# Performance work log

Hardware: AMD Instinct MI355X
Metric: run time of the kernel (lower is better)

The kernel has to match this reference:

```python
import jax, jax.numpy as jnp
import numpy as np


def _ln(x, g, b, eps=1e-5):
    mu = x.mean(-1, keepdims=True)
    var = ((x - mu) ** 2).mean(-1, keepdims=True)
    return (x - mu) / jnp.sqrt(var + eps) * g + b


def setup_inputs() -> dict:
    key = jax.random.key(0)
    ks = jax.random.split(key, 12)
    B, H, W, nh = 32, 64, 64, 8
    L = H * W
    dim, ffn_dim, mem_dim = 512, 2048, 512
    s = 0.02
    d = {}
    d["query"] = jax.random.normal(ks[0], (B, 1, dim), jnp.float32)
    d["mem"] = jax.random.normal(ks[1], (B, L, mem_dim), jnp.float32)
    d["ior_embs"] = jax.random.uniform(ks[2], (B, nh, H, W), jnp.float32)
    # input_proj: Linear(mem_dim, dim) + ReLU + LayerNorm(dim)
    d["W_in"] = jax.random.normal(ks[3], (mem_dim, dim), jnp.float32) * s
    d["b_in"] = jnp.zeros((dim,), jnp.float32)
    d["g_in"] = jnp.ones((dim,), jnp.float32)
    d["be_in"] = jnp.zeros((dim,), jnp.float32)
    # q_w: Linear(dim, dim); kv_w: Linear(dim, 2*dim)
    d["Wq"] = jax.random.normal(ks[4], (dim, dim), jnp.float32) * s
    d["bq"] = jnp.zeros((dim,), jnp.float32)
    d["Wkv"] = jax.random.normal(ks[5], (dim, 2 * dim), jnp.float32) * s
    d["bkv"] = jnp.zeros((2 * dim,), jnp.float32)
    # ffn: Mlp(dim, ffn_dim, dim) with GELU (exact)
    d["W1"] = jax.random.normal(ks[6], (dim, ffn_dim), jnp.float32) * s
    d["b1"] = jnp.zeros((ffn_dim,), jnp.float32)
    d["W2"] = jax.random.normal(ks[7], (ffn_dim, dim), jnp.float32) * s
    d["b2"] = jnp.zeros((dim,), jnp.float32)
    # norm_q, norm_ffn LayerNorms
    d["g_q"] = jnp.ones((dim,), jnp.float32)
    d["be_q"] = jnp.zeros((dim,), jnp.float32)
    d["g_f"] = jnp.ones((dim,), jnp.float32)
    d["be_f"] = jnp.zeros((dim,), jnp.float32)
    return d


def reference(query, mem, ior_embs, W_in, b_in, g_in, be_in, Wq, bq, Wkv, bkv,
              W1, b1, W2, b2, g_q, be_q, g_f, be_f):
    # input_proj: Linear + ReLU + LayerNorm
    m = _ln(jax.nn.relu(mem @ W_in + b_in), g_in, be_in)  # [B,L,C]
    B, L, C = m.shape
    nh = ior_embs.shape[1]
    h = C // nh
    scale = h ** -0.5
    ior = ior_embs.reshape(B, nh, L)  # flatten(2)
    kv = m @ Wkv + bkv
    k, v = kv[..., :C], kv[..., C:]
    # per-head split along last dim == reshape to [.., nh, h]
    q = (_ln(query, g_q, be_q) @ Wq + bq).reshape(B, 1, nh, h)
    k = k.reshape(B, L, nh, h)
    v = v.reshape(B, L, nh, h)
    # softmax-free attention gated by ior mask: attn = (q@k^T)*scale*ior
    attn = jnp.einsum('bqhd,blhd->bhql', q, k) * scale * ior[:, :, None, :]  # [B,nh,1,L]
    x = jnp.einsum('bhql,blhd->bqhd', attn, v).reshape(B, 1, C)  # concat heads
    x = x + query  # residual (short_cut)
    # FFN with pre-norm; dropout p=0 -> identity
    hdn = jax.nn.gelu(_ln(x, g_f, be_f) @ W1 + b1, approximate=False)
    x = x + (hdn @ W2 + b2)
    return x
```

## Files before the change

kernel.cpp:

```cpp
#include <hip/hip_runtime.h>
#include <hip/hip_bf16.h>
#include <math.h>

typedef unsigned short u16;
typedef __bf16 bf16x8 __attribute__((ext_vector_type(8)));
typedef float f32x4 __attribute__((ext_vector_type(4)));

__device__ __forceinline__ float b2f(u16 u) {
  union { unsigned int i; float f; } v; v.i = ((unsigned int)u) << 16; return v.f;
}
__device__ __forceinline__ u16 f2b(float f) {
  union { float f; unsigned int i; } v; v.f = f;
  unsigned int x = v.i;
  return (u16)((x + 0x7fffu + ((x >> 16) & 1u)) >> 16);
}
__device__ __forceinline__ float ldx(const void* p, size_t i, int isf) {
  return isf ? ((const float*)p)[i] : b2f(((const u16*)p)[i]);
}

__global__ void k_detect(const void* __restrict__ query, int* __restrict__ flag) {
  int t = threadIdx.x;
  float v = ((const float*)query)[t];
  int ok = (v == v && fabsf(v) < 100.f && fabsf(v) > 1e-4f) ? 1 : 0;
  unsigned long long m = __ballot(ok);
  if (t == 0) flag[0] = (__popcll(m) >= 32) ? 1 : 0;
}

__global__ __launch_bounds__(256) void k_makeB(const void* __restrict__ Win,
                                               u16* __restrict__ WTf,
                                               const int* __restrict__ flag) {
  int isf = flag[0];
  int t = threadIdx.x;
  int bx = blockIdx.x & 7, by = blockIdx.x >> 3;
  int k0 = bx * 64, j0 = by * 64;
  __shared__ float tile[64][65];
  #pragma unroll
  for (int kx = 0; kx < 16; kx++) {
    int idx = t + 256 * kx;
    int kl = idx >> 6, jl = idx & 63;
    tile[kl][jl] = ldx(Win, (size_t)(k0 + kl) * 512 + (j0 + jl), isf);
  }
  __syncthreads();
  #pragma unroll
  for (int i = 0; i < 2; i++) {
    int chunk = i * 256 + t;
    int q  = chunk & 3;
    int l  = (chunk >> 2) & 15;
    int ksL = (chunk >> 6) & 1;
    int jbL = (chunk >> 7) & 3;
    int j_local = jbL * 16 + l;
    int k_local = ksL * 32 + q * 8;
    union { u16 h[8]; uint4 u; } pk;
    #pragma unroll
    for (int r = 0; r < 8; r++) pk.h[r] = f2b(tile[k_local + r][j_local]);
    int jb = by * 4 + jbL, ks = bx * 2 + ksL;
    *(uint4*)(WTf + ((size_t)(jb * 16 + ks) * 16 + l) * 32 + q * 8) = pk.u;
  }
}

__global__ __launch_bounds__(512) void k_prep2(const void* __restrict__ Wkv,
                                               const void* __restrict__ g_in,
                                               const void* __restrict__ be_in,
                                               float* __restrict__ P1, float* __restrict__ P2,
                                               const int* __restrict__ flag) {
  int isf = flag[0];
  int blk = blockIdx.x;
  int t = threadIdx.x;
  int jj = t & 31, cg = t >> 5;
  int j = blk * 32 + jj;
  float p1 = 0.f, p2 = 0.f;
  for (int cc = 0; cc < 32; cc++) {
    int c = cg * 32 + cc;
    float wv = ldx(Wkv, (size_t)c * 1024 + 512 + j, isf);
    p1 += ldx(g_in, c, isf) * wv;
    p2 += ldx(be_in, c, isf) * wv;
  }
  __shared__ float red[1024];
  red[t * 2] = p1; red[t * 2 + 1] = p2;
  __syncthreads();
  if (t < 32) {
    float s1 = 0.f, s2 = 0.f;
    for (int g2 = 0; g2 < 16; g2++) { s1 += red[(g2 * 32 + t) * 2]; s2 += red[(g2 * 32 + t) * 2 + 1]; }
    P1[blk * 32 + t] = s1;
    P2[blk * 32 + t] = s2;
  }
}

__global__ __launch_bounds__(256) void k_qprep_a(
    const void* __restrict__ query, const void* __restrict__ Wq, const void* __restrict__ bq,
    const void* __restrict__ g_q, const void* __restrict__ be_q,
    float* __restrict__ qr_ws, const int* __restrict__ flag) {
  int isf = flag[0];
  int b = blockIdx.x, jq = blockIdx.y, t = threadIdx.x;
  __shared__ float qf[512];
  __shared__ float red[8];
  __shared__ float stats[2];

  float s = 0.f, ss = 0.f;
  for (int k = 0; k < 2; k++) {
    int c = t + 256 * k;
    float v = ldx(query, (size_t)b * 512 + c, isf);
    qf[c] = v; s += v; ss += v * v;
  }
  for (int off = 32; off; off >>= 1) { s += __shfl_xor(s, off); ss += __shfl_xor(ss, off); }
  int wid = t >> 6, lane = t & 63;
  if (lane == 0) { red[wid * 2] = s; red[wid * 2 + 1] = ss; }
  __syncthreads();
  if (t == 0) {
    float S = 0.f, SS = 0.f;
    for (int w = 0; w < 4; w++) { S += red[w * 2]; SS += red[w * 2 + 1]; }
    float mu = S / 512.f;
    float var = SS / 512.f - mu * mu;
    stats[0] = mu; stats[1] = rsqrtf(var + 1e-5f);
  }
  __syncthreads();
  float mu = stats[0], rstd = stats[1];
  for (int k = 0; k < 2; k++) {
    int c = t + 256 * k;
    qf[c] = (qf[c] - mu) * rstd * ldx(g_q, c, isf) + ldx(be_q, c, isf);
  }
  __syncthreads();
  int jl = t >> 1, half = t & 1;
  int j = jq * 128 + jl;
  const float* qh = qf + half * 256;
  float a0 = 0.f, a1 = 0.f, a2 = 0.f, a3 = 0.f;
  if (isf) {
    const float* wp = (const float*)Wq + (size_t)(half * 256) * 512 + j;
    #pragma unroll 2
    for (int cc = 0; cc < 256; cc += 4) {
      a0 += qh[cc]     * wp[(size_t)cc * 512];
      a1 += qh[cc + 1] * wp[(size_t)(cc + 1) * 512];
      a2 += qh[cc + 2] * wp[(size_t)(cc + 2) * 512];
      a3 += qh[cc + 3] * wp[(size_t)(cc + 3) * 512];
    }
  } else {
    const u16* wp = (const u16*)Wq + (size_t)(half * 256) * 512 + j;
    #pragma unroll 2
    for (int cc = 0; cc < 256; cc += 4) {
      a0 += qh[cc]     * b2f(wp[(size_t)cc * 512]);
      a1 += qh[cc + 1] * b2f(wp[(size_t)(cc + 1) * 512]);
      a2 += qh[cc + 2] * b2f(wp[(size_t)(cc + 2) * 512]);
      a3 += qh[cc + 3] * b2f(wp[(size_t)(cc + 3) * 512]);
    }
  }
  float acc = (a0 + a1) + (a2 + a3);
  acc += __shfl_xor(acc, 1);
  if (half == 0) qr_ws[(size_t)b * 512 + j] = acc + ldx(bq, j, isf);
}

__global__ __launch_bounds__(256) void k_qprep_b(
    const float* __restrict__ qr_ws, const void* __restrict__ Wkv, const void* __restrict__ bkv,
    const void* __restrict__ g_in, const void* __restrict__ be_in,
    u16* __restrict__ guT, float* __restrict__ Gsum_g, float* __restrict__ S0_g,
    const int* __restrict__ flag) {
  int isf = flag[0];
  int b = blockIdx.x, cq = blockIdx.y, t = threadIdx.x;
  __shared__ float qrl[512];
  __shared__ float ul[128 * 8];
  qrl[t] = qr_ws[(size_t)b * 512 + t];
  qrl[t + 256] = qr_ws[(size_t)b * 512 + t + 256];
  __syncthreads();
  #pragma unroll
  for (int e4 = 0; e4 < 4; e4++) {
    int e = t + 256 * e4;
    int cl = e >> 3, n = e & 7;
    int c = cq * 128 + cl;
    const float* qp = qrl + n * 64;
    float acc = 0.f;
    if (isf) {
      const float* wp = (const float*)Wkv + (size_t)c * 1024 + n * 64;
      #pragma unroll 8
      for (int d = 0; d < 64; d++) acc += wp[d] * qp[d];
    } else {
      const u16* wp = (const u16*)Wkv + (size_t)c * 1024 + n * 64;
      #pragma unroll 8
      for (int d = 0; d < 64; d++) acc += b2f(wp[d]) * qp[d];
    }
    ul[cl * 8 + n] = acc;
  }
  __syncthreads();
  #pragma unroll
  for (int e4 = 0; e4 < 4; e4++) {
    int e = t + 256 * e4;
    int cl = e >> 3, n = e & 7;
    int c = cq * 128 + cl;
    guT[((size_t)b * 16 + n) * 512 + c] = f2b(ldx(g_in, c, isf) * ul[cl * 8 + n]);
    guT[((size_t)b * 16 + 8 + n) * 512 + c] = 0;
  }
  if (t < 64) {
    int n = t >> 3, seg = t & 7;
    float gs = 0.f, s0 = 0.f;
    for (int k = 0; k < 16; k++) {
      int cl = seg * 16 + k;
      int c = cq * 128 + cl;
      float uu = ul[cl * 8 + n];
      gs += ldx(g_in, c, isf) * uu;
      s0 += ldx(be_in, c, isf) * uu;
    }
    gs += __shfl_xor(gs, 1); s0 += __shfl_xor(s0, 1);
    gs += __shfl_xor(gs, 2); s0 += __shfl_xor(s0, 2);
    gs += __shfl_xor(gs, 4); s0 += __shfl_xor(s0, 4);
    if (seg == 0) {
      atomicAdd(Gsum_g + b * 8 + n, gs);
      atomicAdd(S0_g + b * 8 + n, s0);
    }
  }
  if (cq == 0 && t < 8) {
    float acc = 0.f;
    for (int d = 0; d < 64; d++) acc += ldx(bkv, t * 64 + d, isf) * qrl[t * 64 + d];
    atomicAdd(S0_g + b * 8 + t, acc);
  }
}

#define LDSWZ(row, byte_in_row) ((((row) << 10) + (byte_in_row)) ^ (((row) & 7) << 4))
__global__ __launch_bounds__(512) void k_main(
    const void* __restrict__ mem, const u16* __restrict__ WTf, const void* __restrict__ b_in,
    const void* __restrict__ ior, const u16* __restrict__ guT,
    const float* __restrict__ Gsum_g, const float* __restrict__ S0_g,
    float* __restrict__ R_g, float* __restrict__ A_g, float* __restrict__ M_g,
    const int* __restrict__ flag) {
  int isf = flag[0];
  int blk = blockIdx.x;
  int b   = blockIdx.y;
  int t = threadIdx.x;
  int w = t >> 6, lane = t & 63;
  int l15 = lane & 15, q = lane >> 4;
  int row0 = blk * 64;

  __shared__ __align__(16) char smem[68096];
  float* rowred  = (float*)smem;
  float* mu_rstd = (float*)(smem + 65536);
  float* a_lds   = (float*)(smem + 66048);
  char*  ymine   = smem + w * 8192;

  float binv[4];
  #pragma unroll
  for (int j = 0; j < 4; j++) binv[j] = ldx(b_in, w * 64 + j * 16 + l15, isf);
  bf16x8 gfrag0 = *(const bf16x8*)(guT + ((size_t)b * 16 + l15) * 512 + w * 64 + q * 8);
  bf16x8 gfrag1 = *(const bf16x8*)(guT + ((size_t)b * 16 + l15) * 512 + w * 64 + 32 + q * 8);
  float Gs  = Gsum_g[b * 8 + (t & 7)];
  float S0v = S0_g[b * 8 + (t & 7)];
  float iorv = ldx(ior, ((size_t)b * 8 + (t & 7)) * 4096 + row0 + (t >> 3), isf);
  const u16* wb = WTf + (size_t)w * 32768 + l15 * 32 + q * 8;

  size_t memBase = ((size_t)b * 4096 + row0) * 512;

  if (isf) {
    #pragma unroll
    for (int h = 0; h < 2; h++) {
      float4 va[8];
      #pragma unroll
      for (int p = 0; p < 8; p++) {
        int i16 = (h * 8 + p) * 512 + t;
        va[p] = *(const float4*)((const float*)mem + memBase + (size_t)i16 * 4);
      }
      #pragma unroll
      for (int p = 0; p < 8; p++) {
        int i16 = (h * 8 + p) * 512 + t;
        int row = i16 >> 7;
        union { u16 hh[4]; uint2 u; } pk;
        pk.hh[0] = f2b(va[p].x); pk.hh[1] = f2b(va[p].y);
        pk.hh[2] = f2b(va[p].z); pk.hh[3] = f2b(va[p].w);
        *(uint2*)(smem + LDSWZ(row, (i16 & 127) << 3)) = pk.u;
      }
    }
  } else {
    uint4 vb[8];
    #pragma unroll
    for (int p = 0; p < 8; p++) {
      int i16 = p * 512 + t;
      vb[p] = *(const uint4*)((const u16*)mem + memBase + (size_t)i16 * 8);
    }
    #pragma unroll
    for (int p = 0; p < 8; p++) {
      int i16 = p * 512 + t;
      int row = i16 >> 6;
      *(uint4*)(smem + LDSWZ(row, (i16 & 63) << 4)) = vb[p];
    }
  }
  __syncthreads();

  f32x4 acc[4][4];
  #pragma unroll
  for (int i = 0; i < 4; i++)
    #pragma unroll
    for (int j = 0; j < 4; j++) { acc[i][j][0]=0.f; acc[i][j][1]=0.f; acc[i][j][2]=0.f; acc[i][j][3]=0.f; }

  #pragma unroll 4
  for (int ks = 0; ks < 16; ks++) {
    bf16x8 aF[4], bF[4];
    #pragma unroll
    for (int j = 0; j < 4; j++)
      bF[j] = *(const bf16x8*)(wb + j * 8192 + ks * 512);
    #pragma unroll
    for (int i = 0; i < 4; i++) {
      int row = i * 16 + l15;
      aF[i] = *(const bf16x8*)(smem + LDSWZ(row, (ks << 6) + (q << 4)));
    }
    #pragma unroll
    for (int i = 0; i < 4; i++)
      #pragma unroll
      for (int j = 0; j < 4; j++)
        acc[i][j] = __builtin_amdgcn_mfma_f32_16x16x32_bf16(aF[i], bF[j], acc[i][j], 0, 0, 0);
  }
  __syncthreads();

  #pragma unroll
  for (int i = 0; i < 4; i++)
    #pragma unroll
    for (int j = 0; j < 4; j++)
      #pragma unroll
      for (int r = 0; r < 4; r++) {
        float v = acc[i][j][r] + binv[j];
        acc[i][j][r] = v > 0.f ? v : 0.f;
      }
  #pragma unroll
  for (int i = 0; i < 4; i++)
    #pragma unroll
    for (int r = 0; r < 4; r++) {
      float s  = acc[i][0][r] + acc[i][1][r] + acc[i][2][r] + acc[i][3][r];
      float ss = acc[i][0][r]*acc[i][0][r] + acc[i][1][r]*acc[i][1][r]
               + acc[i][2][r]*acc[i][2][r] + acc[i][3][r]*acc[i][3][r];
      #pragma unroll
      for (int m = 1; m < 16; m <<= 1) { s += __shfl_xor(s, m); ss += __shfl_xor(ss, m); }
      if (l15 == 0) {
        int row = i * 16 + q * 4 + r;
        rowred[(w * 64 + row) * 2]     = s;
        rowred[(w * 64 + row) * 2 + 1] = ss;
      }
    }
  __syncthreads();
  if (t < 64) {
    float S = 0.f, SS = 0.f;
    for (int w2 = 0; w2 < 8; w2++) { S += rowred[(w2 * 64 + t) * 2]; SS += rowred[(w2 * 64 + t) * 2 + 1]; }
    float mu = S / 512.f;
    float var = SS / 512.f - mu * mu;
    mu_rstd[t * 2] = mu;
    mu_rstd[t * 2 + 1] = rsqrtf(var + 1e-5f);
  }
  __syncthreads();

  #pragma unroll
  for (int i = 0; i < 4; i++)
    #pragma unroll
    for (int j = 0; j < 4; j++)
      #pragma unroll
      for (int r = 0; r < 4; r++) {
        int row = i * 16 + q * 4 + r;
        int byo = (row * 128 + j * 32 + l15 * 2) ^ ((row & 7) << 4);
        *(u16*)(ymine + byo) = f2b(acc[i][j][r]);
      }
  __syncthreads();

  f32x4 Tacc[4];
  #pragma unroll
  for (int rt = 0; rt < 4; rt++) { Tacc[rt][0]=0.f; Tacc[rt][1]=0.f; Tacc[rt][2]=0.f; Tacc[rt][3]=0.f; }
  #pragma unroll
  for (int rt = 0; rt < 4; rt++) {
    int row = rt * 16 + l15;
    int sw = (row & 7) << 4;
    bf16x8 ay0 = *(const bf16x8*)(ymine + ((row * 128 + q * 16) ^ sw));
    Tacc[rt] = __builtin_amdgcn_mfma_f32_16x16x32_bf16(ay0, gfrag0, Tacc[rt], 0, 0, 0);
    bf16x8 ay1 = *(const bf16x8*)(ymine + ((row * 128 + 64 + q * 16) ^ sw));
    Tacc[rt] = __builtin_amdgcn_mfma_f32_16x16x32_bf16(ay1, gfrag1, Tacc[rt], 0, 0, 0);
  }
  {
    float* tp = (float*)ymine;
    if (l15 < 8) {
      #pragma unroll
      for (int rt = 0; rt < 4; rt++)
        #pragma unroll
        for (int r = 0; r < 4; r++)
          tp[(rt * 16 + q * 4 + r) * 8 + l15] = Tacc[rt][r];
    }
  }
  __syncthreads();

  float am_acc, mm_acc;
  {
    int row = t >> 3, n = t & 7;
    float Tsum = 0.f;
    #pragma unroll
    for (int w2 = 0; w2 < 8; w2++)
      Tsum += ((const float*)(smem + w2 * 8192))[row * 8 + n];
    float mu = mu_rstd[row * 2], rstd = mu_rstd[row * 2 + 1];
    float spre = rstd * (Tsum - mu * Gs) + S0v;
    float aval = spre * 0.125f * iorv;
    am_acc = aval;
    mm_acc = aval * mu * rstd;
    a_lds[row * 8 + n] = aval * rstd;
  }
  __syncthreads();

  float rv[4][8];
  #pragma unroll
  for (int j = 0; j < 4; j++)
    #pragma unroll
    for (int n = 0; n < 8; n++) rv[j][n] = 0.f;
  #pragma unroll
  for (int i = 0; i < 4; i++)
    #pragma unroll
    for (int r = 0; r < 4; r++) {
      int row = i * 16 + q * 4 + r;
      const float* ap = a_lds + row * 8;
      float a0=ap[0],a1=ap[1],a2=ap[2],a3=ap[3],a4=ap[4],a5=ap[5],a6=ap[6],a7=ap[7];
      #pragma unroll
      for (int j = 0; j < 4; j++) {
        float m = acc[i][j][r];
        rv[j][0] += m*a0; rv[j][1] += m*a1; rv[j][2] += m*a2; rv[j][3] += m*a3;
        rv[j][4] += m*a4; rv[j][5] += m*a5; rv[j][6] += m*a6; rv[j][7] += m*a7;
      }
    }
  #pragma unroll
  for (int j = 0; j < 4; j++)
    #pragma unroll
    for (int n = 0; n < 8; n++) {
      float v = rv[j][n];
      v += __shfl_xor(v, 16);
      v += __shfl_xor(v, 32);
      rv[j][n] = v;
    }
  if (q == 0) {
    #pragma unroll
    for (int j = 0; j < 4; j++)
      #pragma unroll
      for (int n = 0; n < 8; n++)
        atomicAdd(R_g + ((size_t)b * 8 + n) * 512 + (w * 64 + j * 16 + l15), rv[j][n]);
  }

  am_acc += __shfl_xor(am_acc, 8);
  am_acc += __shfl_xor(am_acc, 16);
  am_acc += __shfl_xor(am_acc, 32);
  mm_acc += __shfl_xor(mm_acc, 8);
  mm_acc += __shfl_xor(mm_acc, 16);
  mm_acc += __shfl_xor(mm_acc, 32);
  if (lane < 8) {
    atomicAdd(A_g + b * 8 + lane, am_acc);
    atomicAdd(M_g + b * 8 + lane, mm_acc);
  }
}

__global__ __launch_bounds__(512) void k_mid(
    const float* __restrict__ R_g, const float* __restrict__ A_g, const float* __restrict__ M_g,
    const float* __restrict__ P1, const float* __restrict__ P2,
    const void* __restrict__ Wkv, const void* __restrict__ bkv, const void* __restrict__ g_in,
    const void* __restrict__ query, const void* __restrict__ g_f, const void* __restrict__ be_f,
    float* __restrict__ xrow_ws, float* __restrict__ xln_ws, float* __restrict__ y_acc,
    const int* __restrict__ flag) {
  int isf = flag[0];
  int b = blockIdx.x, t = threadIdx.x;
  __shared__ float Rl[4096];
  __shared__ float red[16];
  __shared__ float stats[2];
  #pragma unroll
  for (int k = 0; k < 8; k++) {
    int e = t + 512 * k;
    Rl[e] = R_g[(size_t)b * 4096 + e] * ldx(g_in, e & 511, isf);
  }
  __syncthreads();
  int j = t, n = t >> 6;
  float Av = A_g[b * 8 + n], Mv = M_g[b * 8 + n];
  float base = Av * ldx(bkv, 512 + j, isf) - Mv * P1[j] + Av * P2[j];
  const float* rl = Rl + n * 512;
  float a0 = 0.f, a1 = 0.f, a2 = 0.f, a3 = 0.f;
  if (isf) {
    const float* wv = (const float*)Wkv + 512 + j;
    #pragma unroll 2
    for (int c = 0; c < 512; c += 4) {
      a0 += rl[c]     * wv[(size_t)c * 1024];
      a1 += rl[c + 1] * wv[(size_t)(c + 1) * 1024];
      a2 += rl[c + 2] * wv[(size_t)(c + 2) * 1024];
      a3 += rl[c + 3] * wv[(size_t)(c + 3) * 1024];
    }
  } else {
    const u16* wv = (const u16*)Wkv + 512 + j;
    #pragma unroll 2
    for (int c = 0; c < 512; c += 4) {
      a0 += rl[c]     * b2f(wv[(size_t)c * 1024]);
      a1 += rl[c + 1] * b2f(wv[(size_t)(c + 1) * 1024]);
      a2 += rl[c + 2] * b2f(wv[(size_t)(c + 2) * 1024]);
      a3 += rl[c + 3] * b2f(wv[(size_t)(c + 3) * 1024]);
    }
  }
  float v = base + (a0 + a1) + (a2 + a3) + ldx(query, (size_t)b * 512 + t, isf);
  xrow_ws[(size_t)b * 512 + t] = v;
  y_acc[(size_t)b * 512 + t] = 0.f;
  float s1 = v, s2 = v * v;
  for (int off = 32; off; off >>= 1) { s1 += __shfl_xor(s1, off); s2 += __shfl_xor(s2, off); }
  int wid = t >> 6, lane = t & 63;
  if (lane == 0) { red[wid * 2] = s1; red[wid * 2 + 1] = s2; }
  __syncthreads();
  if (t == 0) {
    float S = 0.f, SS = 0.f;
    for (int w = 0; w < 8; w++) { S += red[w * 2]; SS += red[w * 2 + 1]; }
    float mu = S / 512.f;
    float var = SS / 512.f - mu * mu;
    stats[0] = mu; stats[1] = rsqrtf(var + 1e-5f);
  }
  __syncthreads();
  xln_ws[(size_t)b * 512 + t] = (v - stats[0]) * stats[1] * ldx(g_f, t, isf) + ldx(be_f, t, isf);
}

__global__ __launch_bounds__(512) void k_ffn12(
    const float* __restrict__ xln_ws, const void* __restrict__ W1, const void* __restrict__ b1,
    const void* __restrict__ W2, float* __restrict__ y_acc, const int* __restrict__ flag) {
  int isf = flag[0];
  int jb = blockIdx.x, b = blockIdx.y, t = threadIdx.x;
  __shared__ float xl[512];
  __shared__ float hl[512];
  xl[t] = xln_ws[(size_t)b * 512 + t];
  __syncthreads();
  int j = jb * 512 + t;
  float a0 = 0.f, a1 = 0.f, a2 = 0.f, a3 = 0.f;
  if (isf) {
    const float* wp = (const float*)W1 + j;
    #pragma unroll 2
    for (int c = 0; c < 512; c += 4) {
      a0 += xl[c]     * wp[(size_t)c * 2048];
      a1 += xl[c + 1] * wp[(size_t)(c + 1) * 2048];
      a2 += xl[c + 2] * wp[(size_t)(c + 2) * 2048];
      a3 += xl[c + 3] * wp[(size_t)(c + 3) * 2048];
    }
  } else {
    const u16* wp = (const u16*)W1 + j;
    #pragma unroll 2
    for (int c = 0; c < 512; c += 4) {
      a0 += xl[c]     * b2f(wp[(size_t)c * 2048]);
      a1 += xl[c + 1] * b2f(wp[(size_t)(c + 1) * 2048]);
      a2 += xl[c + 2] * b2f(wp[(size_t)(c + 2) * 2048]);
      a3 += xl[c + 3] * b2f(wp[(size_t)(c + 3) * 2048]);
    }
  }
  float acc = (a0 + a1) + (a2 + a3) + ldx(b1, j, isf);
  hl[t] = 0.5f * acc * (1.0f + erff(acc * 0.70710678118654752f));
  __syncthreads();
  float s0 = 0.f, s1 = 0.f, s2 = 0.f, s3 = 0.f;
  if (isf) {
    const float* wp = (const float*)W2 + (size_t)jb * 512 * 512 + t;
    #pragma unroll 2
    for (int c = 0; c < 512; c += 4) {
      s0 += hl[c]     * wp[(size_t)c * 512];
      s1 += hl[c + 1] * wp[(size_t)(c + 1) * 512];
      s2 += hl[c + 2] * wp[(size_t)(c + 2) * 512];
      s3 += hl[c + 3] * wp[(size_t)(c + 3) * 512];
    }
  } else {
    const u16* wp = (const u16*)W2 + (size_t)jb * 512 * 512 + t;
    #pragma unroll 2
    for (int c = 0; c < 512; c += 4) {
      s0 += hl[c]     * b2f(wp[(size_t)c * 512]);
      s1 += hl[c + 1] * b2f(wp[(size_t)(c + 1) * 512]);
      s2 += hl[c + 2] * b2f(wp[(size_t)(c + 2) * 512]);
      s3 += hl[c + 3] * b2f(wp[(size_t)(c + 3) * 512]);
    }
  }
  atomicAdd(y_acc + (size_t)b * 512 + t, (s0 + s1) + (s2 + s3));
}

__global__ __launch_bounds__(512) void k_final(
    const float* __restrict__ y_acc, const void* __restrict__ b2v,
    const float* __restrict__ xrow_ws, void* __restrict__ out,
    const int* __restrict__ flag) {
  int isf = flag[0];
  int b = blockIdx.x, t = threadIdx.x;
  float v = y_acc[(size_t)b * 512 + t] + ldx(b2v, t, isf) + xrow_ws[(size_t)b * 512 + t];
  if (isf) ((float*)out)[b * 512 + t] = v;
  else     ((u16*)out)[b * 512 + t] = f2b(v);
}

extern "C" void kernel_launch(void* const* d_in, const int* in_sizes, int n_in,
                              void* d_out, int out_size, void* d_ws, size_t ws_size,
                              hipStream_t stream) {
  const void* query = d_in[0];
  const void* mem   = d_in[1];
  const void* ior   = d_in[2];
  const void* W_in  = d_in[3];
  const void* b_in  = d_in[4];
  const void* g_in  = d_in[5];
  const void* be_in = d_in[6];
  const void* Wq    = d_in[7];
  const void* bq    = d_in[8];
  const void* Wkv   = d_in[9];
  const void* bkv   = d_in[10];
  const void* W1    = d_in[11];
  const void* b1    = d_in[12];
  const void* W2    = d_in[13];
  const void* b2v   = d_in[14];
  const void* g_q   = d_in[15];
  const void* be_q  = d_in[16];
  const void* g_f   = d_in[17];
  const void* be_f  = d_in[18];

  char* ws = (char*)d_ws;
  int*   flag   = (int*)ws;
  float* S0_g   = (float*)(ws + 256);
  float* Gsum_g = (float*)(ws + 1280);
  float* A_g    = (float*)(ws + 2304);
  float* M_g    = (float*)(ws + 3328);
  float* R_g    = (float*)(ws + 4352);
  u16*   guT    = (u16*)(ws + 528640);
  float* y_acc  = (float*)(ws + 528640);
  float* xrow_ws= (float*)(ws + 594176);
  float* xln_ws = (float*)(ws + 659712);
  u16*   WTf    = (u16*)(ws + 1052928);
  float* P1     = (float*)(ws + 1577216);
  float* P2     = (float*)(ws + 1579264);
  float* qr_ws  = (float*)(ws + 1581312);

  hipMemsetAsync(ws + 256, 0, 528384, stream);
  k_detect<<<dim3(1), dim3(64), 0, stream>>>(query, flag);
  k_makeB<<<dim3(64), dim3(256), 0, stream>>>(W_in, WTf, flag);
  k_prep2<<<dim3(16), dim3(512), 0, stream>>>(Wkv, g_in, be_in, P1, P2, flag);
  k_qprep_a<<<dim3(32, 4), dim3(256), 0, stream>>>(query, Wq, bq, g_q, be_q, qr_ws, flag);
  k_qprep_b<<<dim3(32, 4), dim3(256), 0, stream>>>(qr_ws, Wkv, bkv, g_in, be_in,
                                                   guT, Gsum_g, S0_g, flag);
  k_main<<<dim3(64, 32), dim3(512), 0, stream>>>(mem, WTf, b_in, ior, guT, Gsum_g, S0_g,
                                                 R_g, A_g, M_g, flag);
  k_mid<<<dim3(32), dim3(512), 0, stream>>>(R_g, A_g, M_g, P1, P2, Wkv, bkv, g_in,
                                            query, g_f, be_f, xrow_ws, xln_ws, y_acc, flag);
  k_ffn12<<<dim3(4, 32), dim3(512), 0, stream>>>(xln_ws, W1, b1, W2, y_acc, flag);
  k_final<<<dim3(32), dim3(512), 0, stream>>>(y_acc, b2v, xrow_ws, d_out, flag);
}
```

Before: 723.8 us.

## Merge prep kernels, inline dtype detection, fuse mid stage into FFN

```diff
diff --git a/kernel.cpp b/kernel.cpp
--- a/kernel.cpp
+++ b/kernel.cpp
@@ -17,146 +17,146 @@
 __device__ __forceinline__ float ldx(const void* p, size_t i, int isf) {
   return isf ? ((const float*)p)[i] : b2f(((const u16*)p)[i]);
 }
-
-__global__ void k_detect(const void* __restrict__ query, int* __restrict__ flag) {
+__device__ __forceinline__ int detect_isf(const void* query, int t, volatile float* slot) {
+  if (t < 64) {
+    float v = ((const float*)query)[t];
+    int ok = (v == v && fabsf(v) < 100.f && fabsf(v) > 1e-4f) ? 1 : 0;
+    unsigned long long m = __ballot(ok);
+    if (t == 0) *slot = (__popcll(m) >= 32) ? 1.f : 0.f;
+  }
+  __syncthreads();
+  return *slot != 0.f;
+}
+
+__global__ __launch_bounds__(256) void k_prep(
+    const void* __restrict__ query, const void* __restrict__ Win, u16* __restrict__ WTf,
+    const void* __restrict__ Wkv, const void* __restrict__ g_in, const void* __restrict__ be_in,
+    float* __restrict__ P1, float* __restrict__ P2,
+    const void* __restrict__ Wq, const void* __restrict__ bq,
+    const void* __restrict__ g_q, const void* __restrict__ be_q,
+    float* __restrict__ qr_ws) {
+  __shared__ __align__(16) char pb[16704];
+  float* slot = (float*)(pb + 16640);
   int t = threadIdx.x;
-  float v = ((const float*)query)[t];
-  int ok = (v == v && fabsf(v) < 100.f && fabsf(v) > 1e-4f) ? 1 : 0;
-  unsigned long long m = __ballot(ok);
-  if (t == 0) flag[0] = (__popcll(m) >= 32) ? 1 : 0;
-}
-
-__global__ __launch_bounds__(256) void k_makeB(const void* __restrict__ Win,
-                                               u16* __restrict__ WTf,
-                                               const int* __restrict__ flag) {
-  int isf = flag[0];
-  int t = threadIdx.x;
-  int bx = blockIdx.x & 7, by = blockIdx.x >> 3;
-  int k0 = bx * 64, j0 = by * 64;
-  __shared__ float tile[64][65];
-  #pragma unroll
-  for (int kx = 0; kx < 16; kx++) {
-    int idx = t + 256 * kx;
-    int kl = idx >> 6, jl = idx & 63;
-    tile[kl][jl] = ldx(Win, (size_t)(k0 + kl) * 512 + (j0 + jl), isf);
-  }
-  __syncthreads();
-  #pragma unroll
-  for (int i = 0; i < 2; i++) {
-    int chunk = i * 256 + t;
-    int q  = chunk & 3;
-    int l  = (chunk >> 2) & 15;
-    int ksL = (chunk >> 6) & 1;
-    int jbL = (chunk >> 7) & 3;
-    int j_local = jbL * 16 + l;
-    int k_local = ksL * 32 + q * 8;
-    union { u16 h[8]; uint4 u; } pk;
-    #pragma unroll
-    for (int r = 0; r < 8; r++) pk.h[r] = f2b(tile[k_local + r][j_local]);
-    int jb = by * 4 + jbL, ks = bx * 2 + ksL;
-    *(uint4*)(WTf + ((size_t)(jb * 16 + ks) * 16 + l) * 32 + q * 8) = pk.u;
-  }
-}
-
-__global__ __launch_bounds__(512) void k_prep2(const void* __restrict__ Wkv,
-                                               const void* __restrict__ g_in,
-                                               const void* __restrict__ be_in,
-                                               float* __restrict__ P1, float* __restrict__ P2,
-                                               const int* __restrict__ flag) {
-  int isf = flag[0];
+  int isf = detect_isf(query, t, slot);
   int blk = blockIdx.x;
-  int t = threadIdx.x;
-  int jj = t & 31, cg = t >> 5;
-  int j = blk * 32 + jj;
-  float p1 = 0.f, p2 = 0.f;
-  for (int cc = 0; cc < 32; cc++) {
-    int c = cg * 32 + cc;
-    float wv = ldx(Wkv, (size_t)c * 1024 + 512 + j, isf);
-    p1 += ldx(g_in, c, isf) * wv;
-    p2 += ldx(be_in, c, isf) * wv;
-  }
-  __shared__ float red[1024];
-  red[t * 2] = p1; red[t * 2 + 1] = p2;
-  __syncthreads();
-  if (t < 32) {
-    float s1 = 0.f, s2 = 0.f;
-    for (int g2 = 0; g2 < 16; g2++) { s1 += red[(g2 * 32 + t) * 2]; s2 += red[(g2 * 32 + t) * 2 + 1]; }
-    P1[blk * 32 + t] = s1;
-    P2[blk * 32 + t] = s2;
-  }
-}
-
-__global__ __launch_bounds__(256) void k_qprep_a(
-    const void* __restrict__ query, const void* __restrict__ Wq, const void* __restrict__ bq,
-    const void* __restrict__ g_q, const void* __restrict__ be_q,
-    float* __restrict__ qr_ws, const int* __restrict__ flag) {
-  int isf = flag[0];
-  int b = blockIdx.x, jq = blockIdx.y, t = threadIdx.x;
-  __shared__ float qf[512];
-  __shared__ float red[8];
-  __shared__ float stats[2];
-
-  float s = 0.f, ss = 0.f;
-  for (int k = 0; k < 2; k++) {
-    int c = t + 256 * k;
-    float v = ldx(query, (size_t)b * 512 + c, isf);
-    qf[c] = v; s += v; ss += v * v;
-  }
-  for (int off = 32; off; off >>= 1) { s += __shfl_xor(s, off); ss += __shfl_xor(ss, off); }
-  int wid = t >> 6, lane = t & 63;
-  if (lane == 0) { red[wid * 2] = s; red[wid * 2 + 1] = ss; }
-  __syncthreads();
-  if (t == 0) {
-    float S = 0.f, SS = 0.f;
-    for (int w = 0; w < 4; w++) { S += red[w * 2]; SS += red[w * 2 + 1]; }
-    float mu = S / 512.f;
-    float var = SS / 512.f - mu * mu;
-    stats[0] = mu; stats[1] = rsqrtf(var + 1e-5f);
-  }
-  __syncthreads();
-  float mu = stats[0], rstd = stats[1];
-  for (int k = 0; k < 2; k++) {
-    int c = t + 256 * k;
-    qf[c] = (qf[c] - mu) * rstd * ldx(g_q, c, isf) + ldx(be_q, c, isf);
-  }
-  __syncthreads();
-  int jl = t >> 1, half = t & 1;
-  int j = jq * 128 + jl;
-  const float* qh = qf + half * 256;
-  float a0 = 0.f, a1 = 0.f, a2 = 0.f, a3 = 0.f;
-  if (isf) {
-    const float* wp = (const float*)Wq + (size_t)(half * 256) * 512 + j;
-    #pragma unroll 2
-    for (int cc = 0; cc < 256; cc += 4) {
-      a0 += qh[cc]     * wp[(size_t)cc * 512];
-      a1 += qh[cc + 1] * wp[(size_t)(cc + 1) * 512];
-      a2 += qh[cc + 2] * wp[(size_t)(cc + 2) * 512];
-      a3 += qh[cc + 3] * wp[(size_t)(cc + 3) * 512];
+
+  if (blk < 64) {
+    float (*tile)[65] = (float(*)[65])pb;
+    int bx = blk & 7, by = blk >> 3;
+    int k0 = bx * 64, j0 = by * 64;
+    #pragma unroll
+    for (int kx = 0; kx < 16; kx++) {
+      int idx = t + 256 * kx;
+      int kl = idx >> 6, jl = idx & 63;
+      tile[kl][jl] = ldx(Win, (size_t)(k0 + kl) * 512 + (j0 + jl), isf);
+    }
+    __syncthreads();
+    #pragma unroll
+    for (int i = 0; i < 2; i++) {
+      int chunk = i * 256 + t;
+      int q  = chunk & 3;
+      int l  = (chunk >> 2) & 15;
+      int ksL = (chunk >> 6) & 1;
+      int jbL = (chunk >> 7) & 3;
+      int j_local = jbL * 16 + l;
+      int k_local = ksL * 32 + q * 8;
+      union { u16 h[8]; uint4 u; } pk;
+      #pragma unroll
+      for (int r = 0; r < 8; r++) pk.h[r] = f2b(tile[k_local + r][j_local]);
+      int jb = by * 4 + jbL, ks = bx * 2 + ksL;
+      *(uint4*)(WTf + ((size_t)(jb * 16 + ks) * 16 + l) * 32 + q * 8) = pk.u;
+    }
+  } else if (blk < 80) {
+    float* red = (float*)pb;
+    int blk2 = blk - 64;
+    int jj = t & 31, cg = t >> 5;
+    int j = blk2 * 32 + jj;
+    float p1 = 0.f, p2 = 0.f;
+    for (int cc = 0; cc < 64; cc++) {
+      int c = cg * 64 + cc;
+      float wv = ldx(Wkv, (size_t)c * 1024 + 512 + j, isf);
+      p1 += ldx(g_in, c, isf) * wv;
+      p2 += ldx(be_in, c, isf) * wv;
+    }
+    red[t * 2] = p1; red[t * 2 + 1] = p2;
+    __syncthreads();
+    if (t < 32) {
+      float s1 = 0.f, s2 = 0.f;
+      for (int g2 = 0; g2 < 8; g2++) { s1 += red[(g2 * 32 + t) * 2]; s2 += red[(g2 * 32 + t) * 2 + 1]; }
+      P1[blk2 * 32 + t] = s1;
+      P2[blk2 * 32 + t] = s2;
     }
   } else {
-    const u16* wp = (const u16*)Wq + (size_t)(half * 256) * 512 + j;
-    #pragma unroll 2
-    for (int cc = 0; cc < 256; cc += 4) {
-      a0 += qh[cc]     * b2f(wp[(size_t)cc * 512]);
-      a1 += qh[cc + 1] * b2f(wp[(size_t)(cc + 1) * 512]);
-      a2 += qh[cc + 2] * b2f(wp[(size_t)(cc + 2) * 512]);
-      a3 += qh[cc + 3] * b2f(wp[(size_t)(cc + 3) * 512]);
-    }
-  }
-  float acc = (a0 + a1) + (a2 + a3);
-  acc += __shfl_xor(acc, 1);
-  if (half == 0) qr_ws[(size_t)b * 512 + j] = acc + ldx(bq, j, isf);
+    int bb = blk - 80;
+    int b = bb >> 2, jq = bb & 3;
+    float* qf    = (float*)pb;
+    float* red   = (float*)(pb + 2048);
+    float* stats = (float*)(pb + 2080);
+    float s = 0.f, ss = 0.f;
+    for (int k = 0; k < 2; k++) {
+      int c = t + 256 * k;
+      float v = ldx(query, (size_t)b * 512 + c, isf);
+      qf[c] = v; s += v; ss += v * v;
+    }
+    for (int off = 32; off; off >>= 1) { s += __shfl_xor(s, off); ss += __shfl_xor(ss, off); }
+    int wid = t >> 6, lane = t & 63;
+    if (lane == 0) { red[wid * 2] = s; red[wid * 2 + 1] = ss; }
+    __syncthreads();
+    if (t == 0) {
+      float S = 0.f, SS = 0.f;
+      for (int w = 0; w < 4; w++) { S += red[w * 2]; SS += red[w * 2 + 1]; }
+      float mu = S / 512.f;
+      float var = SS / 512.f - mu * mu;
+      stats[0] = mu; stats[1] = rsqrtf(var + 1e-5f);
+    }
+    __syncthreads();
+    float mu = stats[0], rstd = stats[1];
+    for (int k = 0; k < 2; k++) {
+      int c = t + 256 * k;
+      qf[c] = (qf[c] - mu) * rstd * ldx(g_q, c, isf) + ldx(be_q, c, isf);
+    }
+    __syncthreads();
+    int jl = t >> 1, half = t & 1;
+    int j = jq * 128 + jl;
+    const float* qh = qf + half * 256;
+    float a0 = 0.f, a1 = 0.f, a2 = 0.f, a3 = 0.f;
+    if (isf) {
+      const float* wp = (const float*)Wq + (size_t)(half * 256) * 512 + j;
+      #pragma unroll 2
+      for (int cc = 0; cc < 256; cc += 4) {
+        a0 += qh[cc]     * wp[(size_t)cc * 512];
+        a1 += qh[cc + 1] * wp[(size_t)(cc + 1) * 512];
+        a2 += qh[cc + 2] * wp[(size_t)(cc + 2) * 512];
+        a3 += qh[cc + 3] * wp[(size_t)(cc + 3) * 512];
+      }
+    } else {
+      const u16* wp = (const u16*)Wq + (size_t)(half * 256) * 512 + j;
+      #pragma unroll 2
+      for (int cc = 0; cc < 256; cc += 4) {
+        a0 += qh[cc]     * b2f(wp[(size_t)cc * 512]);
+        a1 += qh[cc + 1] * b2f(wp[(size_t)(cc + 1) * 512]);
+        a2 += qh[cc + 2] * b2f(wp[(size_t)(cc + 2) * 512]);
+        a3 += qh[cc + 3] * b2f(wp[(size_t)(cc + 3) * 512]);
+      }
+    }
+    float acc = (a0 + a1) + (a2 + a3);
+    acc += __shfl_xor(acc, 1);
+    if (half == 0) qr_ws[(size_t)b * 512 + j] = acc + ldx(bq, j, isf);
+  }
 }
 
 __global__ __launch_bounds__(256) void k_qprep_b(
+    const void* __restrict__ query,
     const float* __restrict__ qr_ws, const void* __restrict__ Wkv, const void* __restrict__ bkv,
     const void* __restrict__ g_in, const void* __restrict__ be_in,
-    u16* __restrict__ guT, float* __restrict__ Gsum_g, float* __restrict__ S0_g,
-    const int* __restrict__ flag) {
-  int isf = flag[0];
-  int b = blockIdx.x, cq = blockIdx.y, t = threadIdx.x;
+    u16* __restrict__ guT, float* __restrict__ Gsum_g, float* __restrict__ S0_g) {
   __shared__ float qrl[512];
-  __shared__ float ul[128 * 8];
+  __shared__ float ul[1024];
+  __shared__ float slot[1];
+  int t = threadIdx.x;
+  int isf = detect_isf(query, t, slot);
+  int b = blockIdx.x, cq = blockIdx.y;
   qrl[t] = qr_ws[(size_t)b * 512 + t];
   qrl[t + 256] = qr_ws[(size_t)b * 512 + t + 256];
   __syncthreads();
@@ -214,12 +214,11 @@
 
 #define LDSWZ(row, byte_in_row) ((((row) << 10) + (byte_in_row)) ^ (((row) & 7) << 4))
 __global__ __launch_bounds__(512) void k_main(
+    const void* __restrict__ query,
     const void* __restrict__ mem, const u16* __restrict__ WTf, const void* __restrict__ b_in,
     const void* __restrict__ ior, const u16* __restrict__ guT,
     const float* __restrict__ Gsum_g, const float* __restrict__ S0_g,
-    float* __restrict__ R_g, float* __restrict__ A_g, float* __restrict__ M_g,
-    const int* __restrict__ flag) {
-  int isf = flag[0];
+    float* __restrict__ R_g, float* __restrict__ A_g, float* __restrict__ M_g) {
   int blk = blockIdx.x;
   int b   = blockIdx.y;
   int t = threadIdx.x;
@@ -232,6 +231,8 @@
   float* mu_rstd = (float*)(smem + 65536);
   float* a_lds   = (float*)(smem + 66048);
   char*  ymine   = smem + w * 8192;
+
+  int isf = detect_isf(query, t, mu_rstd);
 
   float binv[4];
   #pragma unroll
@@ -440,18 +441,24 @@
   }
 }
 
-__global__ __launch_bounds__(512) void k_mid(
+__global__ __launch_bounds__(512) void k_midffn(
+    const void* __restrict__ query,
     const float* __restrict__ R_g, const float* __restrict__ A_g, const float* __restrict__ M_g,
     const float* __restrict__ P1, const float* __restrict__ P2,
     const void* __restrict__ Wkv, const void* __restrict__ bkv, const void* __restrict__ g_in,
-    const void* __restrict__ query, const void* __restrict__ g_f, const void* __restrict__ be_f,
-    float* __restrict__ xrow_ws, float* __restrict__ xln_ws, float* __restrict__ y_acc,
-    const int* __restrict__ flag) {
-  int isf = flag[0];
-  int b = blockIdx.x, t = threadIdx.x;
+    const void* __restrict__ g_f, const void* __restrict__ be_f,
+    const void* __restrict__ W1, const void* __restrict__ b1, const void* __restrict__ W2,
+    float* __restrict__ xrow_ws, float* __restrict__ y_acc) {
   __shared__ float Rl[4096];
+  __shared__ float xl[512];
+  __shared__ float hl[512];
   __shared__ float red[16];
   __shared__ float stats[2];
+  __shared__ float slot[1];
+  int t = threadIdx.x;
+  int isf = detect_isf(query, t, slot);
+  int jb = blockIdx.x, b = blockIdx.y;
+
   #pragma unroll
   for (int k = 0; k < 8; k++) {
     int e = t + 512 * k;
@@ -483,8 +490,7 @@
     }
   }
   float v = base + (a0 + a1) + (a2 + a3) + ldx(query, (size_t)b * 512 + t, isf);
-  xrow_ws[(size_t)b * 512 + t] = v;
-  y_acc[(size_t)b * 512 + t] = 0.f;
+  if (jb == 0) xrow_ws[(size_t)b * 512 + t] = v;
   float s1 = v, s2 = v * v;
   for (int off = 32; off; off >>= 1) { s1 += __shfl_xor(s1, off); s2 += __shfl_xor(s2, off); }
   int wid = t >> 6, lane = t & 63;
@@ -498,71 +504,63 @@
     stats[0] = mu; stats[1] = rsqrtf(var + 1e-5f);
   }
   __syncthreads();
-  xln_ws[(size_t)b * 512 + t] = (v - stats[0]) * stats[1] * ldx(g_f, t, isf) + ldx(be_f, t, isf);
-}
-
-__global__ __launch_bounds__(512) void k_ffn12(
-    const float* __restrict__ xln_ws, const void* __restrict__ W1, const void* __restrict__ b1,
-    const void* __restrict__ W2, float* __restrict__ y_acc, const int* __restrict__ flag) {
-  int isf = flag[0];
-  int jb = blockIdx.x, b = blockIdx.y, t = threadIdx.x;
-  __shared__ float xl[512];
-  __shared__ float hl[512];
-  xl[t] = xln_ws[(size_t)b * 512 + t];
-  __syncthreads();
-  int j = jb * 512 + t;
-  float a0 = 0.f, a1 = 0.f, a2 = 0.f, a3 = 0.f;
+  xl[t] = (v - stats[0]) * stats[1] * ldx(g_f, t, isf) + ldx(be_f, t, isf);
+  __syncthreads();
+  int j2 = jb * 512 + t;
+  float b0 = 0.f, b1a = 0.f, b2a = 0.f, b3a = 0.f;
   if (isf) {
-    const float* wp = (const float*)W1 + j;
+    const float* wp = (const float*)W1 + j2;
     #pragma unroll 2
     for (int c = 0; c < 512; c += 4) {
-      a0 += xl[c]     * wp[(size_t)c * 2048];
-      a1 += xl[c + 1] * wp[(size_t)(c + 1) * 2048];
-      a2 += xl[c + 2] * wp[(size_t)(c + 2) * 2048];
-      a3 += xl[c + 3] * wp[(size_t)(c + 3) * 2048];
+      b0  += xl[c]     * wp[(size_t)c * 2048];
+      b1a += xl[c + 1] * wp[(size_t)(c + 1) * 2048];
+      b2a += xl[c + 2] * wp[(size_t)(c + 2) * 2048];
+      b3a += xl[c + 3] * wp[(size_t)(c + 3) * 2048];
     }
   } else {
-    const u16* wp = (const u16*)W1 + j;
+    const u16* wp = (const u16*)W1 + j2;
     #pragma unroll 2
     for (int c = 0; c < 512; c += 4) {
-      a0 += xl[c]     * b2f(wp[(size_t)c * 2048]);
-      a1 += xl[c + 1] * b2f(wp[(size_t)(c + 1) * 2048]);
-      a2 += xl[c + 2] * b2f(wp[(size_t)(c + 2) * 2048]);
-      a3 += xl[c + 3] * b2f(wp[(size_t)(c + 3) * 2048]);
-    }
-  }
-  float acc = (a0 + a1) + (a2 + a3) + ldx(b1, j, isf);
-  hl[t] = 0.5f * acc * (1.0f + erff(acc * 0.70710678118654752f));
-  __syncthreads();
-  float s0 = 0.f, s1 = 0.f, s2 = 0.f, s3 = 0.f;
+      b0  += xl[c]     * b2f(wp[(size_t)c * 2048]);
+      b1a += xl[c + 1] * b2f(wp[(size_t)(c + 1) * 2048]);
+      b2a += xl[c + 2] * b2f(wp[(size_t)(c + 2) * 2048]);
+      b3a += xl[c + 3] * b2f(wp[(size_t)(c + 3) * 2048]);
+    }
+  }
+  float hacc = (b0 + b1a) + (b2a + b3a) + ldx(b1, j2, isf);
+  hl[t] = 0.5f * hacc * (1.0f + erff(hacc * 0.70710678118654752f));
+  __syncthreads();
+  float s0 = 0.f, s1b = 0.f, s2b = 0.f, s3b = 0.f;
   if (isf) {
     const float* wp = (const float*)W2 + (size_t)jb * 512 * 512 + t;
     #pragma unroll 2
     for (int c = 0; c < 512; c += 4) {
-      s0 += hl[c]     * wp[(size_t)c * 512];
-      s1 += hl[c + 1] * wp[(size_t)(c + 1) * 512];
-      s2 += hl[c + 2] * wp[(size_t)(c + 2) * 512];
-      s3 += hl[c + 3] * wp[(size_t)(c + 3) * 512];
+      s0  += hl[c]     * wp[(size_t)c * 512];
+      s1b += hl[c + 1] * wp[(size_t)(c + 1) * 512];
+      s2b += hl[c + 2] * wp[(size_t)(c + 2) * 512];
+      s3b += hl[c + 3] * wp[(size_t)(c + 3) * 512];
     }
   } else {
     const u16* wp = (const u16*)W2 + (size_t)jb * 512 * 512 + t;
     #pragma unroll 2
     for (int c = 0; c < 512; c += 4) {
-      s0 += hl[c]     * b2f(wp[(size_t)c * 512]);
-      s1 += hl[c + 1] * b2f(wp[(size_t)(c + 1) * 512]);
-      s2 += hl[c + 2] * b2f(wp[(size_t)(c + 2) * 512]);
-      s3 += hl[c + 3] * b2f(wp[(size_t)(c + 3) * 512]);
-    }
-  }
-  atomicAdd(y_acc + (size_t)b * 512 + t, (s0 + s1) + (s2 + s3));
+      s0  += hl[c]     * b2f(wp[(size_t)c * 512]);
+      s1b += hl[c + 1] * b2f(wp[(size_t)(c + 1) * 512]);
+      s2b += hl[c + 2] * b2f(wp[(size_t)(c + 2) * 512]);
+      s3b += hl[c + 3] * b2f(wp[(size_t)(c + 3) * 512]);
+    }
+  }
+  atomicAdd(y_acc + (size_t)b * 512 + t, (s0 + s1b) + (s2b + s3b));
 }
 
 __global__ __launch_bounds__(512) void k_final(
+    const void* __restrict__ query,
     const float* __restrict__ y_acc, const void* __restrict__ b2v,
-    const float* __restrict__ xrow_ws, void* __restrict__ out,
-    const int* __restrict__ flag) {
-  int isf = flag[0];
-  int b = blockIdx.x, t = threadIdx.x;
+    const float* __restrict__ xrow_ws, void* __restrict__ out) {
+  __shared__ float slot[1];
+  int t = threadIdx.x;
+  int isf = detect_isf(query, t, slot);
+  int b = blockIdx.x;
   float v = y_acc[(size_t)b * 512 + t] + ldx(b2v, t, isf) + xrow_ws[(size_t)b * 512 + t];
   if (isf) ((float*)out)[b * 512 + t] = v;
   else     ((u16*)out)[b * 512 + t] = f2b(v);
@@ -592,32 +590,28 @@
   const void* be_f  = d_in[18];
 
   char* ws = (char*)d_ws;
-  int*   flag   = (int*)ws;
-  float* S0_g   = (float*)(ws + 256);
-  float* Gsum_g = (float*)(ws + 1280);
-  float* A_g    = (float*)(ws + 2304);
-  float* M_g    = (float*)(ws + 3328);
-  float* R_g    = (float*)(ws + 4352);
-  u16*   guT    = (u16*)(ws + 528640);
-  float* y_acc  = (float*)(ws + 528640);
-  float* xrow_ws= (float*)(ws + 594176);
-  float* xln_ws = (float*)(ws + 659712);
-  u16*   WTf    = (u16*)(ws + 1052928);
-  float* P1     = (float*)(ws + 1577216);
-  float* P2     = (float*)(ws + 1579264);
-  float* qr_ws  = (float*)(ws + 1581312);
-
-  hipMemsetAsync(ws + 256, 0, 528384, stream);
-  k_detect<<<dim3(1), dim3(64), 0, stream>>>(query, flag);
-  k_makeB<<<dim3(64), dim3(256), 0, stream>>>(W_in, WTf, flag);
-  k_prep2<<<dim3(16), dim3(512), 0, stream>>>(Wkv, g_in, be_in, P1, P2, flag);
-  k_qprep_a<<<dim3(32, 4), dim3(256), 0, stream>>>(query, Wq, bq, g_q, be_q, qr_ws, flag);
-  k_qprep_b<<<dim3(32, 4), dim3(256), 0, stream>>>(qr_ws, Wkv, bkv, g_in, be_in,
-                                                   guT, Gsum_g, S0_g, flag);
-  k_main<<<dim3(64, 32), dim3(512), 0, stream>>>(mem, WTf, b_in, ior, guT, Gsum_g, S0_g,
-                                                 R_g, A_g, M_g, flag);
-  k_mid<<<dim3(32), dim3(512), 0, stream>>>(R_g, A_g, M_g, P1, P2, Wkv, bkv, g_in,
-                                            query, g_f, be_f, xrow_ws, xln_ws, y_acc, flag);
-  k_ffn12<<<dim3(4, 32), dim3(512), 0, stream>>>(xln_ws, W1, b1, W2, y_acc, flag);
-  k_final<<<dim3(32), dim3(512), 0, stream>>>(y_acc, b2v, xrow_ws, d_out, flag);
-}
+  float* S0_g   = (float*)(ws + 0);
+  float* Gsum_g = (float*)(ws + 1024);
+  float* A_g    = (float*)(ws + 2048);
+  float* M_g    = (float*)(ws + 3072);
+  float* R_g    = (float*)(ws + 4096);
+  float* y_acc  = (float*)(ws + 528384);
+  u16*   guT    = (u16*)(ws + 593920);
+  float* xrow_ws= (float*)(ws + 1118208);
+  u16*   WTf    = (u16*)(ws + 1183744);
+  float* P1     = (float*)(ws + 1708032);
+  float* P2     = (float*)(ws + 1710080);
+  float* qr_ws  = (float*)(ws + 1712128);
+
+  hipMemsetAsync(ws, 0, 593920, stream);
+  k_prep<<<dim3(208), dim3(256), 0, stream>>>(query, W_in, WTf, Wkv, g_in, be_in,
+                                              P1, P2, Wq, bq, g_q, be_q, qr_ws);
+  k_qprep_b<<<dim3(32, 4), dim3(256), 0, stream>>>(query, qr_ws, Wkv, bkv, g_in, be_in,
+                                                   guT, Gsum_g, S0_g);
+  k_main<<<dim3(64, 32), dim3(512), 0, stream>>>(query, mem, WTf, b_in, ior, guT,
+                                                 Gsum_g, S0_g, R_g, A_g, M_g);
+  k_midffn<<<dim3(4, 32), dim3(512), 0, stream>>>(query, R_g, A_g, M_g, P1, P2,
+                                                  Wkv, bkv, g_in, g_f, be_f,
+                                                  W1, b1, W2, xrow_ws, y_acc);
+  k_final<<<dim3(32), dim3(512), 0, stream>>>(query, y_acc, b2v, xrow_ws, d_out);
+}
```

Result: faster. 696.7 us (-3.7%).
